# Performance work log

Measured on AMD Instinct MI355X. Metric: run time of the kernel, lower is better.

The kernel has to match this reference:

```python
import jax, jax.numpy as jnp
import numpy as np

GRID_SIZE = (256, 256, 256, 4)
N_POINTS = 2_000_000


def _corner_offsets(dims):
    # All 2^dims binary offsets in 'ij' meshgrid order, matching tf.meshgrid(..., indexing='ij')
    grids = np.meshgrid(*([np.arange(2)] * dims), indexing='ij')
    return jnp.asarray(np.stack([g.reshape(-1) for g in grids], axis=1), dtype=jnp.float32)  # [2^d, d]


def setup_inputs() -> dict:
    key = jax.random.key(0)
    k1, k2 = jax.random.split(key)
    input_coordinates = jax.random.uniform(k1, (N_POINTS, 3), dtype=jnp.float32)
    field = jax.random.uniform(k2, GRID_SIZE, dtype=jnp.float32)
    return {"input_coordinates": input_coordinates, "field": field}


def reference(input_coordinates, field):
    dims = field.ndim - 1  # spatial dims (channel dim last), = 3 here
    spatial = jnp.asarray(field.shape[:-1], dtype=jnp.float32)
    x = input_coordinates * spatial                 # [N, d] grid-space coords
    fl = jnp.floor(x)
    offsets = _corner_offsets(dims)                 # [2^d, d]
    corners = fl[None, :, :] + offsets[:, None, :]  # [2^d, N, d]
    # Clip indices to valid range (jax gather clip mode; ceil can hit the boundary)
    max_idx = jnp.asarray(field.shape[:-1], dtype=jnp.int32) - 1
    idx = jnp.clip(corners.astype(jnp.int32), 0, max_idx)
    vals = field[tuple(jnp.moveaxis(idx, -1, 0))]   # [2^d, N, C] gather at each corner
    # Faithful to source: weight for each corner is prod_d |corner_d - x_d|
    w = jnp.prod(jnp.abs(corners - x[None, :, :]), axis=-1)  # [2^d, N]
    out = jnp.sum(vals * w[..., None], axis=0)      # [N, C]
    return jax.nn.relu(out)
```

## Files before the change

kernel.cpp:

```cpp
#include <hip/hip_runtime.h>


#define SPATIAL 256
#define CHANNELS 4

__global__ __launch_bounds__(256) void relu_field_kernel(
    const float* __restrict__ coords,
    const float* __restrict__ field,
    float* __restrict__ out,
    int n)
{
    int i = blockIdx.x * blockDim.x + threadIdx.x;
    if (i >= n) return;

    const float cx = coords[3 * i + 0] * (float)SPATIAL;
    const float cy = coords[3 * i + 1] * (float)SPATIAL;
    const float cz = coords[3 * i + 2] * (float)SPATIAL;

    const float flx = floorf(cx), fly = floorf(cy), flz = floorf(cz);
    const float fx = cx - flx, fy = cy - fly, fz = cz - flz;

    int ix0 = (int)flx, iy0 = (int)fly, iz0 = (int)flz;
    ix0 = min(max(ix0, 0), SPATIAL - 1);
    iy0 = min(max(iy0, 0), SPATIAL - 1);
    iz0 = min(max(iz0, 0), SPATIAL - 1);
    const int ix1 = min(ix0 + 1, SPATIAL - 1);
    const int iy1 = min(iy0 + 1, SPATIAL - 1);
    const int iz1 = min(iz0 + 1, SPATIAL - 1);

    const float wx0 = fx, wx1 = 1.0f - fx;
    const float wy0 = fy, wy1 = 1.0f - fy;
    const float wz0 = fz, wz1 = 1.0f - fz;

    const long b00 = ((long)ix0 * SPATIAL + iy0) * SPATIAL;
    const long b01 = ((long)ix0 * SPATIAL + iy1) * SPATIAL;
    const long b10 = ((long)ix1 * SPATIAL + iy0) * SPATIAL;
    const long b11 = ((long)ix1 * SPATIAL + iy1) * SPATIAL;

    const float4* __restrict__ f4 = reinterpret_cast<const float4*>(field);

    const float4 v000 = f4[b00 + iz0];
    const float4 v001 = f4[b00 + iz1];
    const float4 v010 = f4[b01 + iz0];
    const float4 v011 = f4[b01 + iz1];
    const float4 v100 = f4[b10 + iz0];
    const float4 v101 = f4[b10 + iz1];
    const float4 v110 = f4[b11 + iz0];
    const float4 v111 = f4[b11 + iz1];

    const float w000 = wx0 * wy0 * wz0;
    const float w001 = wx0 * wy0 * wz1;
    const float w010 = wx0 * wy1 * wz0;
    const float w011 = wx0 * wy1 * wz1;
    const float w100 = wx1 * wy0 * wz0;
    const float w101 = wx1 * wy0 * wz1;
    const float w110 = wx1 * wy1 * wz0;
    const float w111 = wx1 * wy1 * wz1;

    float4 acc;
    acc.x = v000.x * w000; acc.y = v000.y * w000; acc.z = v000.z * w000; acc.w = v000.w * w000;
    acc.x += v001.x * w001; acc.y += v001.y * w001; acc.z += v001.z * w001; acc.w += v001.w * w001;
    acc.x += v010.x * w010; acc.y += v010.y * w010; acc.z += v010.z * w010; acc.w += v010.w * w010;
    acc.x += v011.x * w011; acc.y += v011.y * w011; acc.z += v011.z * w011; acc.w += v011.w * w011;
    acc.x += v100.x * w100; acc.y += v100.y * w100; acc.z += v100.z * w100; acc.w += v100.w * w100;
    acc.x += v101.x * w101; acc.y += v101.y * w101; acc.z += v101.z * w101; acc.w += v101.w * w101;
    acc.x += v110.x * w110; acc.y += v110.y * w110; acc.z += v110.z * w110; acc.w += v110.w * w110;
    acc.x += v111.x * w111; acc.y += v111.y * w111; acc.z += v111.z * w111; acc.w += v111.w * w111;

    acc.x = fmaxf(acc.x, 0.0f);
    acc.y = fmaxf(acc.y, 0.0f);
    acc.z = fmaxf(acc.z, 0.0f);
    acc.w = fmaxf(acc.w, 0.0f);

    reinterpret_cast<float4*>(out)[i] = acc;
}

extern "C" void kernel_launch(void* const* d_in, const int* in_sizes, int n_in,
                              void* d_out, int out_size, void* d_ws, size_t ws_size,
                              hipStream_t stream) {
    const float* coords = (const float*)d_in[0];
    const float* field  = (const float*)d_in[1];
    float* out          = (float*)d_out;

    const int n = in_sizes[0] / 3;
    const int block = 256;
    const int grid = (n + block - 1) / block;
    relu_field_kernel<<<grid, block, 0, stream>>>(coords, field, out, n);
}
```

Before: 473.1 us.

## Bucket-sort points by spatial cell before trilinear gather for cache locality

Adds a counting sort of the query points into 8x8x8 spatial buckets: a histogram, a multi-level prefix scan, and an atomic scatter into a workspace buffer. The gather kernel then processes points in bucket order so that neighbouring threads read nearby field voxels. This targets cache misses from random gathers into the 1 GiB field. In exchange it adds several extra kernel launches, atomics and extra memory traffic for the sorted buffer, and the output is written in scattered order. It falls back to the original kernel when the workspace is too small.

New measurement: 654.8 us. +38.4%, slower.

```diff
diff --git a/kernel.cpp b/kernel.cpp
--- a/kernel.cpp
+++ b/kernel.cpp
@@ -2,28 +2,93 @@
 
 
 #define SPATIAL 256
-#define CHANNELS 4
+#define NBUCK   32768
+#define SCAN_BLK 256
+#define NAUX    128
 
-__global__ __launch_bounds__(256) void relu_field_kernel(
-    const float* __restrict__ coords,
-    const float* __restrict__ field,
-    float* __restrict__ out,
-    int n)
+__device__ __forceinline__ int bucket_of(float cx, float cy, float cz) {
+    int ix = min(max((int)floorf(cx), 0), SPATIAL - 1);
+    int iy = min(max((int)floorf(cy), 0), SPATIAL - 1);
+    int iz = min(max((int)floorf(cz), 0), SPATIAL - 1);
+    return ((ix >> 3) << 10) | ((iy >> 3) << 5) | (iz >> 3);
+}
+
+__global__ __launch_bounds__(256) void hist_kernel(
+    const float* __restrict__ coords, int* __restrict__ hist, int n)
 {
     int i = blockIdx.x * blockDim.x + threadIdx.x;
     if (i >= n) return;
+    float cx = coords[3 * i + 0] * (float)SPATIAL;
+    float cy = coords[3 * i + 1] * (float)SPATIAL;
+    float cz = coords[3 * i + 2] * (float)SPATIAL;
+    atomicAdd(&hist[bucket_of(cx, cy, cz)], 1);
+}
 
-    const float cx = coords[3 * i + 0] * (float)SPATIAL;
-    const float cy = coords[3 * i + 1] * (float)SPATIAL;
-    const float cz = coords[3 * i + 2] * (float)SPATIAL;
+__global__ __launch_bounds__(SCAN_BLK) void scan_local(
+    int* __restrict__ hist, int* __restrict__ aux)
+{
+    __shared__ int tmp[SCAN_BLK];
+    int t = threadIdx.x;
+    int base = blockIdx.x * SCAN_BLK;
+    int v = hist[base + t];
+    tmp[t] = v;
+    __syncthreads();
+    for (int off = 1; off < SCAN_BLK; off <<= 1) {
+        int x = (t >= off) ? tmp[t - off] : 0;
+        __syncthreads();
+        tmp[t] += x;
+        __syncthreads();
+    }
+    hist[base + t] = tmp[t] - v;
+    if (t == SCAN_BLK - 1) aux[blockIdx.x] = tmp[t];
+}
 
+__global__ __launch_bounds__(NAUX) void scan_aux(int* __restrict__ aux)
+{
+    __shared__ int tmp[NAUX];
+    int t = threadIdx.x;
+    int v = aux[t];
+    tmp[t] = v;
+    __syncthreads();
+    for (int off = 1; off < NAUX; off <<= 1) {
+        int x = (t >= off) ? tmp[t - off] : 0;
+        __syncthreads();
+        tmp[t] += x;
+        __syncthreads();
+    }
+    aux[t] = tmp[t] - v;
+}
+
+__global__ __launch_bounds__(SCAN_BLK) void add_offsets(
+    int* __restrict__ hist, const int* __restrict__ aux)
+{
+    hist[blockIdx.x * SCAN_BLK + threadIdx.x] += aux[blockIdx.x];
+}
+
+__global__ __launch_bounds__(256) void scatter_kernel(
+    const float* __restrict__ coords, int* __restrict__ hist,
+    float4* __restrict__ sorted, int n)
+{
+    int i = blockIdx.x * blockDim.x + threadIdx.x;
+    if (i >= n) return;
+    float cx = coords[3 * i + 0] * (float)SPATIAL;
+    float cy = coords[3 * i + 1] * (float)SPATIAL;
+    float cz = coords[3 * i + 2] * (float)SPATIAL;
+    int pos = atomicAdd(&hist[bucket_of(cx, cy, cz)], 1);
+    float4 s;
+    s.x = cx; s.y = cy; s.z = cz; s.w = __int_as_float(i);
+    sorted[pos] = s;
+}
+
+__device__ __forceinline__ float4 interp_point(
+    float cx, float cy, float cz, const float4* __restrict__ f4)
+{
     const float flx = floorf(cx), fly = floorf(cy), flz = floorf(cz);
     const float fx = cx - flx, fy = cy - fly, fz = cz - flz;
 
-    int ix0 = (int)flx, iy0 = (int)fly, iz0 = (int)flz;
-    ix0 = min(max(ix0, 0), SPATIAL - 1);
-    iy0 = min(max(iy0, 0), SPATIAL - 1);
-    iz0 = min(max(iz0, 0), SPATIAL - 1);
+    int ix0 = min(max((int)flx, 0), SPATIAL - 1);
+    int iy0 = min(max((int)fly, 0), SPATIAL - 1);
+    int iz0 = min(max((int)flz, 0), SPATIAL - 1);
     const int ix1 = min(ix0 + 1, SPATIAL - 1);
     const int iy1 = min(iy0 + 1, SPATIAL - 1);
     const int iz1 = min(iz0 + 1, SPATIAL - 1);
@@ -36,8 +101,6 @@
     const long b01 = ((long)ix0 * SPATIAL + iy1) * SPATIAL;
     const long b10 = ((long)ix1 * SPATIAL + iy0) * SPATIAL;
     const long b11 = ((long)ix1 * SPATIAL + iy1) * SPATIAL;
-
-    const float4* __restrict__ f4 = reinterpret_cast<const float4*>(field);
 
     const float4 v000 = f4[b00 + iz0];
     const float4 v001 = f4[b00 + iz1];
@@ -71,7 +134,33 @@
     acc.y = fmaxf(acc.y, 0.0f);
     acc.z = fmaxf(acc.z, 0.0f);
     acc.w = fmaxf(acc.w, 0.0f);
+    return acc;
+}
 
+__global__ __launch_bounds__(256) void gather_kernel(
+    const float4* __restrict__ sorted, const float* __restrict__ field,
+    float* __restrict__ out, int n)
+{
+    int i = blockIdx.x * blockDim.x + threadIdx.x;
+    if (i >= n) return;
+    float4 s = sorted[i];
+    int orig = __float_as_int(s.w);
+    float4 acc = interp_point(s.x, s.y, s.z,
+                              reinterpret_cast<const float4*>(field));
+    reinterpret_cast<float4*>(out)[orig] = acc;
+}
+
+__global__ __launch_bounds__(256) void relu_field_kernel(
+    const float* __restrict__ coords, const float* __restrict__ field,
+    float* __restrict__ out, int n)
+{
+    int i = blockIdx.x * blockDim.x + threadIdx.x;
+    if (i >= n) return;
+    float cx = coords[3 * i + 0] * (float)SPATIAL;
+    float cy = coords[3 * i + 1] * (float)SPATIAL;
+    float cz = coords[3 * i + 2] * (float)SPATIAL;
+    float4 acc = interp_point(cx, cy, cz,
+                              reinterpret_cast<const float4*>(field));
     reinterpret_cast<float4*>(out)[i] = acc;
 }
 
@@ -85,5 +174,26 @@
     const int n = in_sizes[0] / 3;
     const int block = 256;
     const int grid = (n + block - 1) / block;
-    relu_field_kernel<<<grid, block, 0, stream>>>(coords, field, out, n);
+
+    const size_t histBytes = (size_t)NBUCK * 4;
+    const size_t auxBytes  = 512;
+    const size_t need = histBytes + auxBytes + (size_t)n * 16;
+
+    if (ws_size < need) {
+        relu_field_kernel<<<grid, block, 0, stream>>>(coords, field, out, n);
+        return;
+    }
+
+    char* w = (char*)d_ws;
+    int*    hist   = (int*)w;
+    int*    aux    = (int*)(w + histBytes);
+    float4* sorted = (float4*)(w + histBytes + auxBytes);
+
+    hipMemsetAsync(hist, 0, histBytes, stream);
+    hist_kernel   <<<grid, block, 0, stream>>>(coords, hist, n);
+    scan_local    <<<NAUX, SCAN_BLK, 0, stream>>>(hist, aux);
+    scan_aux      <<<1, NAUX, 0, stream>>>(aux);
+    add_offsets   <<<NAUX, SCAN_BLK, 0, stream>>>(hist, aux);
+    scatter_kernel<<<grid, block, 0, stream>>>(coords, hist, sorted, n);
+    gather_kernel <<<grid, block, 0, stream>>>(sorted, field, out, n);
 }
```
